# Kernel optimization log

Hardware: AMD Instinct MI355X
Metric: run time of the kernel (lower is better)

Reference implementation:

```python
import jax, jax.numpy as jnp
import numpy as np

L_MAX = 6
R = 1
IN_IRREPS  = [(256,0),(128,1),(128,2),(64,3),(64,4),(64,5),(64,6)]
HID_IRREPS = [(64,0),(64,1),(64,2),(32,3),(32,4),(32,5),(32,6)]
N_SCALARS = 64
N_GATES = sum(m for m, l in HID_IRREPS if l > 0)  # 256
PRE_IRREPS = [(N_SCALARS,0),(N_GATES,0)] + [(m,l) for m,l in HID_IRREPS if l > 0]
OUT_IRREPS = [(R,l) for l in range(L_MAX+1)]

def _dim(irr):
    return sum(m*(2*l+1) for m, l in irr)

def _wsize(in_irr, out_irr):
    mul_in = {l: m for m, l in in_irr}
    return sum(mul_in[l]*mo for mo, l in out_irr)

def e3linear(x, wflat, in_irr, out_irr):
    # block-diagonal per-irrep linear with e3nn 1/sqrt(fan_in) normalization
    B = x.shape[0]
    blocks = {}
    off = 0
    for mul, l in in_irr:
        d = mul*(2*l+1)
        blocks[l] = (x[:, off:off+d].reshape(B, mul, 2*l+1), mul)
        off += d
    outs = []
    woff = 0
    for mul_out, l in out_irr:
        xb, mul_in = blocks[l]
        w = wflat[woff:woff+mul_in*mul_out].reshape(mul_in, mul_out)
        woff += mul_in*mul_out
        y = jnp.einsum('bim,io->bom', xb, w) * (1.0/np.sqrt(mul_in))
        outs.append(y.reshape(B, mul_out*(2*l+1)))
    return jnp.concatenate(outs, axis=1)

def gate(z):
    # z = [scalars 64x0e | gates 256x0e | gated l>0 irreps]
    s = jax.nn.silu(z[:, :N_SCALARS])
    g = jax.nn.sigmoid(z[:, N_SCALARS:N_SCALARS+N_GATES])
    x = z[:, N_SCALARS+N_GATES:]
    outs = [s]
    goff = 0
    xoff = 0
    for mul, l in HID_IRREPS:
        if l == 0:
            continue
        m = 2*l+1
        xb = x[:, xoff:xoff+mul*m].reshape(-1, mul, m)
        outs.append((xb * g[:, goff:goff+mul, None]).reshape(-1, mul*m))
        goff += mul
        xoff += mul*m
    return jnp.concatenate(outs, axis=1)

def _forward(v_raw, w1, w2, w3, w4):
    x = gate(e3linear(v_raw, w1, IN_IRREPS, PRE_IRREPS))
    x = gate(e3linear(x, w2, HID_IRREPS, PRE_IRREPS))
    x = gate(e3linear(x, w3, HID_IRREPS, PRE_IRREPS))
    c = e3linear(x, w4, HID_IRREPS, OUT_IRREPS)  # [B, 49]
    B = c.shape[0]
    segs = []
    off = 0
    for l in range(L_MAX+1):
        m = 2*l+1
        seg = c[:, off:off+R*m].reshape(B, R, m).transpose(0, 2, 1)  # (B, m, R)
        segs.append(seg)
        off += R*m
    return jnp.concatenate(segs, axis=1)  # (B, 49, R)

def setup_inputs():
    key = jax.random.key(0)
    ks = jax.random.split(key, 5)
    B = 16384
    return {
        "v_raw": jax.random.normal(ks[0], (B, _dim(IN_IRREPS)), jnp.float32),
        "w1": jax.random.normal(ks[1], (_wsize(IN_IRREPS, PRE_IRREPS),), jnp.float32),
        "w2": jax.random.normal(ks[2], (_wsize(HID_IRREPS, PRE_IRREPS),), jnp.float32),
        "w3": jax.random.normal(ks[3], (_wsize(HID_IRREPS, PRE_IRREPS),), jnp.float32),
        "w4": jax.random.normal(ks[4], (_wsize(HID_IRREPS, OUT_IRREPS),), jnp.float32),
    }

def reference(v_raw, w1, w2, w3, w4):
    return _forward(v_raw, w1, w2, w3, w4)
```

## Files before the change

### kernel.cpp

```cpp
#include <hip/hip_runtime.h>
#include <cstddef>


typedef _Float16 half8 __attribute__((ext_vector_type(8)));
typedef _Float16 half4 __attribute__((ext_vector_type(4)));
typedef float    f32x4 __attribute__((ext_vector_type(4)));
typedef float    fvec4 __attribute__((ext_vector_type(4)));
typedef unsigned int u32x4 __attribute__((ext_vector_type(4)));

#define B_ROWS   16
#define IN_DIM   3840
#define OUT_COLS 49
#define GP  264
#define HSP 72

#define OFF_G1  0
#define OFF_G2  4224
#define OFF_G3  8448
#define OFF_HS1 12672
#define OFF_HS2 13824
#define SMEM_ELTS 14976

#define P2BASE 106496
#define P3BASE 139264

__global__ __launch_bounds__(256) void prep_weights(
    const float* __restrict__ w1, const float* __restrict__ w2,
    const float* __restrict__ w3, _Float16* __restrict__ packed)
{
  static const int K_[24]    = {256,256,128,128,64,64,64,64,  64,64,64,64,32,32,32,32,
                                64,64,64,64,32,32,32,32};
  static const int N_[24]    = {64,256,64,64,32,32,32,32,  64,256,64,64,32,32,32,32,
                                64,256,64,64,32,32,32,32};
  static const int woff_[24] = {0,16384,81920,90112,98304,100352,102400,104448,
                                0,4096,20480,24576,28672,29696,30720,31744,
                                0,4096,20480,24576,28672,29696,30720,31744};
  static const int poff_[24] = {0,16384,81920,90112,98304,100352,102400,104448,
                                106496,110592,126976,131072,135168,136192,137216,138240,
                                139264,143360,159744,163840,167936,168960,169984,171008};
  const int g = blockIdx.x * 256 + threadIdx.x;
  int bi = 0;
#pragma unroll
  for (int i = 1; i < 24; ++i) if (g * 8 >= poff_[i]) bi = i;
  const float* w = (bi < 8) ? w1 : ((bi < 16) ? w2 : w3);
  const int rel8 = g - poff_[bi] / 8;
  const int lane = rel8 & 63;
  const int fi   = rel8 >> 6;
  const int K = K_[bi], N = N_[bi];
  const int KF = K >> 5;
  const int kf = fi % KF;
  const int mt = fi / KF;
  const int k0 = kf * 32 + (lane >> 4) * 8;
  const int o  = mt * 16 + (lane & 15);
  const float scale = 1.0f / sqrtf((float)K);
  half8 vv;
#pragma unroll
  for (int j = 0; j < 8; ++j)
    vv[j] = (_Float16)(w[woff_[bi] + (size_t)(k0 + j) * N + o] * scale);
  *(half8*)(packed + (size_t)g * 8) = vv;
}

template<int L> struct CP {
  static constexpr int TWOL1 = 2 * L + 1;
  static constexpr int K1  = (L <= 2) ? 128 : 64;
  static constexpr int N1  = (L <= 2) ? 64  : 32;
  static constexpr int KF1 = K1 / 32;
  static constexpr int KF2 = N1 / 32;
  static constexpr int MT  = N1 / 16;
  static constexpr int INOFF = (L==1)?256:(L==2)?640:(L==3)?1280:(L==4)?1728:(L==5)?2304:3008;
  static constexpr int P1    = (L==1)?81920:(L==2)?90112:(L==3)?98304:(L==4)?100352:(L==5)?102400:104448;
  static constexpr int P2R   = (L==1)?20480:(L==2)?24576:(L==3)?28672:(L==4)?29696:(L==5)?30720:31744;
  static constexpr int GO    = (L==1)?0:(L==2)?64:(L==3)?128:(L==4)?160:(L==5)?192:224;
  static constexpr int W4O   = (L==1)?64:(L==2)?128:(L==3)?192:(L==4)?224:(L==5)?256:288;
  static constexpr float SCALE = (N1 == 64) ? 0.125f : 0.17677669529663687f;
};

__device__ __forceinline__ unsigned pack2(float x, float y)
{
  const unsigned short lo = __builtin_bit_cast(unsigned short, (_Float16)x);
  const unsigned short hi = __builtin_bit_cast(unsigned short, (_Float16)y);
  return ((unsigned)hi << 16) | (unsigned)lo;
}

template<int MT>
__device__ __forceinline__ void exchange(const unsigned (&p)[MT][2],
                                         half8 (&bv)[MT / 2])
{
  const int lane  = threadIdx.x & 63;
  const int addrA = (((lane & 15) + ((lane & 16) << 1)) << 2);
  const int addrB = addrA + 64;
  const bool useHi = (lane & 32) != 0;
#pragma unroll
  for (int h = 0; h < MT / 2; ++h) {
    const int a0 = __builtin_amdgcn_ds_bpermute(addrA, (int)p[2 * h][0]);
    const int a1 = __builtin_amdgcn_ds_bpermute(addrA, (int)p[2 * h][1]);
    const int a2 = __builtin_amdgcn_ds_bpermute(addrA, (int)p[2 * h + 1][0]);
    const int a3 = __builtin_amdgcn_ds_bpermute(addrA, (int)p[2 * h + 1][1]);
    const int b0 = __builtin_amdgcn_ds_bpermute(addrB, (int)p[2 * h][0]);
    const int b1 = __builtin_amdgcn_ds_bpermute(addrB, (int)p[2 * h][1]);
    const int b2 = __builtin_amdgcn_ds_bpermute(addrB, (int)p[2 * h + 1][0]);
    const int b3 = __builtin_amdgcn_ds_bpermute(addrB, (int)p[2 * h + 1][1]);
    u32x4 w;
    w[0] = (unsigned)(useHi ? a2 : a0);
    w[1] = (unsigned)(useHi ? a3 : a1);
    w[2] = (unsigned)(useHi ? b2 : b0);
    w[3] = (unsigned)(useHi ? b3 : b1);
    bv[h] = __builtin_bit_cast(half8, w);
  }
}

template<int L>
__device__ __forceinline__ void unit_load(const float* __restrict__ vraw,
                                          int b0, int ct, float (&rg)[CP<L>::KF1 * 8])
{
  using P = CP<L>;
  const int lane = threadIdx.x & 63;
  const int col  = lane & 15;
  const int quad = lane >> 4;
  const int c = ct * 16 + col;
  const int b = c / P::TWOL1;
  const int m = c - b * P::TWOL1;
  const float* base = vraw + (size_t)(b0 + b) * IN_DIM + P::INOFF + m
                    + (size_t)(quad * 8) * P::TWOL1;
#pragma unroll
  for (int kf = 0; kf < P::KF1; ++kf)
#pragma unroll
    for (int j = 0; j < 8; ++j)
      rg[kf * 8 + j] = base[(size_t)(kf * 32 + j) * P::TWOL1];
}

template<int L>
__device__ __forceinline__ void unit_compute(
    const float (&rg)[CP<L>::KF1 * 8], const _Float16* __restrict__ pk,
    const _Float16* G1, const _Float16* G2, const _Float16* G3,
    const float* __restrict__ w4, float* __restrict__ out, int b0, int ct)
{
  using P = CP<L>;
  const int lane = threadIdx.x & 63;
  const int col  = lane & 15;
  const int quad = lane >> 4;
  const int c = ct * 16 + col;
  const int b = c / P::TWOL1;
  const int m = c - b * P::TWOL1;
  half8 bf[P::KF1];
#pragma unroll
  for (int kf = 0; kf < P::KF1; ++kf)
#pragma unroll
    for (int j = 0; j < 8; ++j) bf[kf][j] = (_Float16)rg[kf * 8 + j];

  unsigned p1[P::MT][2];
#pragma unroll
  for (int mt = 0; mt < P::MT; ++mt) {
    f32x4 acc = {0.f, 0.f, 0.f, 0.f};
#pragma unroll
    for (int kf = 0; kf < P::KF1; ++kf) {
      const half8 av = *(const half8*)(pk + P::P1 + (size_t)((mt * P::KF1 + kf) * 64 + lane) * 8);
      acc = __builtin_amdgcn_mfma_f32_16x16x32_f16(av, bf[kf], acc, 0, 0, 0);
    }
    const int o0 = mt * 16 + quad * 4;
    const half4 g4 = *(const half4*)(G1 + b * GP + P::GO + o0);
    p1[mt][0] = pack2(acc[0] * (float)g4[0], acc[1] * (float)g4[1]);
    p1[mt][1] = pack2(acc[2] * (float)g4[2], acc[3] * (float)g4[3]);
  }
  half8 bv2[P::KF2];
  exchange<P::MT>(p1, bv2);

  unsigned p2[P::MT][2];
#pragma unroll
  for (int mt = 0; mt < P::MT; ++mt) {
    f32x4 acc = {0.f, 0.f, 0.f, 0.f};
#pragma unroll
    for (int kf = 0; kf < P::KF2; ++kf) {
      const half8 av = *(const half8*)(pk + P2BASE + P::P2R + (size_t)((mt * P::KF2 + kf) * 64 + lane) * 8);
      acc = __builtin_amdgcn_mfma_f32_16x16x32_f16(av, bv2[kf], acc, 0, 0, 0);
    }
    const int o0 = mt * 16 + quad * 4;
    const half4 g4 = *(const half4*)(G2 + b * GP + P::GO + o0);
    p2[mt][0] = pack2(acc[0] * (float)g4[0], acc[1] * (float)g4[1]);
    p2[mt][1] = pack2(acc[2] * (float)g4[2], acc[3] * (float)g4[3]);
  }
  half8 bv3[P::KF2];
  exchange<P::MT>(p2, bv3);

  float s = 0.f;
#pragma unroll
  for (int mt = 0; mt < P::MT; ++mt) {
    f32x4 acc = {0.f, 0.f, 0.f, 0.f};
#pragma unroll
    for (int kf = 0; kf < P::KF2; ++kf) {
      const half8 av = *(const half8*)(pk + P3BASE + P::P2R + (size_t)((mt * P::KF2 + kf) * 64 + lane) * 8);
      acc = __builtin_amdgcn_mfma_f32_16x16x32_f16(av, bv3[kf], acc, 0, 0, 0);
    }
    const int o0 = mt * 16 + quad * 4;
    const half4 g4 = *(const half4*)(G3 + b * GP + P::GO + o0);
#pragma unroll
    for (int r = 0; r < 4; ++r)
      s += acc[r] * (float)g4[r] * w4[P::W4O + o0 + r];
  }
  s += __shfl_xor(s, 16, 64);
  s += __shfl_xor(s, 32, 64);
  if (quad == 0)
    out[(size_t)(b0 + b) * OUT_COLS + L * L + m] = s * P::SCALE;
}

template<int L, int CT0, int NCT>
__device__ __forceinline__ void run_chain(
    const float* __restrict__ vraw, const _Float16* __restrict__ pk,
    const _Float16* G1, const _Float16* G2, const _Float16* G3,
    const float* __restrict__ w4, float* __restrict__ out, int b0)
{
  float rg[2][CP<L>::KF1 * 8];
  unit_load<L>(vraw, b0, CT0, rg[0]);
#pragma unroll
  for (int u = 0; u < NCT; ++u) {
    if (u + 1 < NCT) unit_load<L>(vraw, b0, CT0 + u + 1, rg[(u + 1) & 1]);
    unit_compute<L>(rg[u & 1], pk, G1, G2, G3, w4, out, b0, CT0 + u);
  }
}

template<int L, int CT0, int NCT>
__device__ __forceinline__ void run_chain_pre(
    const float* __restrict__ vraw, const _Float16* __restrict__ pk,
    const _Float16* G1, const _Float16* G2, const _Float16* G3,
    const float* __restrict__ w4, float* __restrict__ out, int b0,
    const float (&pre)[CP<L>::KF1 * 8])
{
  float rg[2][CP<L>::KF1 * 8];
#pragma unroll
  for (int i = 0; i < CP<L>::KF1 * 8; ++i) rg[0][i] = pre[i];
#pragma unroll
  for (int u = 0; u < NCT; ++u) {
    if (u + 1 < NCT) unit_load<L>(vraw, b0, CT0 + u + 1, rg[(u + 1) & 1]);
    unit_compute<L>(rg[u & 1], pk, G1, G2, G3, w4, out, b0, CT0 + u);
  }
}

__device__ __forceinline__ void load_scal_frags(const float* __restrict__ vraw,
                                                int b0, half8 (&sf)[8])
{
  const int lane = threadIdx.x & 63;
  const int col  = lane & 15;
  const int quad = lane >> 4;
  const float* base = vraw + (size_t)(b0 + col) * IN_DIM + quad * 8;
#pragma unroll
  for (int kf = 0; kf < 8; ++kf) {
    const fvec4 a = *(const fvec4*)(base + kf * 32);
    const fvec4 b2 = *(const fvec4*)(base + kf * 32 + 4);
#pragma unroll
    for (int j = 0; j < 4; ++j) { sf[kf][j] = (_Float16)a[j]; sf[kf][4 + j] = (_Float16)b2[j]; }
  }
}

__device__ __forceinline__ void scal_L1(const half8 (&sf)[8],
    const _Float16* __restrict__ pk, _Float16* Hs1, _Float16* G1v)
{
  const int lane = threadIdx.x & 63;
  const int wv   = threadIdx.x >> 6;
  const int col  = lane & 15;
  const int quad = lane >> 4;
  {
    f32x4 acc = {0.f, 0.f, 0.f, 0.f};
#pragma unroll
    for (int kf = 0; kf < 8; ++kf) {
      const half8 av = *(const half8*)(pk + (size_t)((wv * 8 + kf) * 64 + lane) * 8);
      acc = __builtin_amdgcn_mfma_f32_16x16x32_f16(av, sf[kf], acc, 0, 0, 0);
    }
    const int o0 = wv * 16 + quad * 4;
    half4 h;
#pragma unroll
    for (int r = 0; r < 4; ++r) { const float z = acc[r]; h[r] = (_Float16)(z / (1.f + __expf(-z))); }
    *(half4*)(Hs1 + col * HSP + o0) = h;
  }
#pragma unroll
  for (int t = 0; t < 4; ++t) {
    const int mt = wv * 4 + t;
    f32x4 acc = {0.f, 0.f, 0.f, 0.f};
#pragma unroll
    for (int kf = 0; kf < 8; ++kf) {
      const half8 av = *(const half8*)(pk + 16384 + (size_t)((mt * 8 + kf) * 64 + lane) * 8);
      acc = __builtin_amdgcn_mfma_f32_16x16x32_f16(av, sf[kf], acc, 0, 0, 0);
    }
    const int o0 = mt * 16 + quad * 4;
    half4 g;
#pragma unroll
    for (int r = 0; r < 4; ++r) g[r] = (_Float16)(1.f / (1.f + __expf(-acc[r])));
    *(half4*)(G1v + col * GP + o0) = g;
  }
}

__device__ __forceinline__ void scal_mid(const _Float16* HsIn,
    const _Float16* __restrict__ pkS, const _Float16* __restrict__ pkG,
    _Float16* HsOut, _Float16* Gv)
{
  const int lane = threadIdx.x & 63;
  const int wv   = threadIdx.x >> 6;
  const int col  = lane & 15;
  const int quad = lane >> 4;
  half8 bf[2];
#pragma unroll
  for (int kf = 0; kf < 2; ++kf)
    bf[kf] = *(const half8*)(HsIn + col * HSP + kf * 32 + quad * 8);
  {
    f32x4 acc = {0.f, 0.f, 0.f, 0.f};
#pragma unroll
    for (int kf = 0; kf < 2; ++kf) {
      const half8 av = *(const half8*)(pkS + (size_t)((wv * 2 + kf) * 64 + lane) * 8);
      acc = __builtin_amdgcn_mfma_f32_16x16x32_f16(av, bf[kf], acc, 0, 0, 0);
    }
    const int o0 = wv * 16 + quad * 4;
    half4 h;
#pragma unroll
    for (int r = 0; r < 4; ++r) { const float z = acc[r]; h[r] = (_Float16)(z / (1.f + __expf(-z))); }
    *(half4*)(HsOut + col * HSP + o0) = h;
  }
#pragma unroll
  for (int t = 0; t < 4; ++t) {
    const int mt = wv * 4 + t;
    f32x4 acc = {0.f, 0.f, 0.f, 0.f};
#pragma unroll
    for (int kf = 0; kf < 2; ++kf) {
      const half8 av = *(const half8*)(pkG + (size_t)((mt * 2 + kf) * 64 + lane) * 8);
      acc = __builtin_amdgcn_mfma_f32_16x16x32_f16(av, bf[kf], acc, 0, 0, 0);
    }
    const int o0 = mt * 16 + quad * 4;
    half4 g;
#pragma unroll
    for (int r = 0; r < 4; ++r) g[r] = (_Float16)(1.f / (1.f + __expf(-acc[r])));
    *(half4*)(Gv + col * GP + o0) = g;
  }
}

__device__ __forceinline__ void scal_last(const _Float16* Hs2,
    const _Float16* __restrict__ pkS, const _Float16* __restrict__ pkG,
    _Float16* G3v, const float* __restrict__ w4, float* __restrict__ out, int b0)
{
  const int lane = threadIdx.x & 63;
  const int wv   = threadIdx.x >> 6;
  const int col  = lane & 15;
  const int quad = lane >> 4;
  half8 bf[2];
#pragma unroll
  for (int kf = 0; kf < 2; ++kf)
    bf[kf] = *(const half8*)(Hs2 + col * HSP + kf * 32 + quad * 8);
  if (wv == 0) {
    float s = 0.f;
#pragma unroll
    for (int mt = 0; mt < 4; ++mt) {
      f32x4 acc = {0.f, 0.f, 0.f, 0.f};
#pragma unroll
      for (int kf = 0; kf < 2; ++kf) {
        const half8 av = *(const half8*)(pkS + (size_t)((mt * 2 + kf) * 64 + lane) * 8);
        acc = __builtin_amdgcn_mfma_f32_16x16x32_f16(av, bf[kf], acc, 0, 0, 0);
      }
      const int o0 = mt * 16 + quad * 4;
#pragma unroll
      for (int r = 0; r < 4; ++r) {
        const float z = acc[r];
        s += (z / (1.f + __expf(-z))) * w4[o0 + r];
      }
    }
    s += __shfl_xor(s, 16, 64);
    s += __shfl_xor(s, 32, 64);
    if (quad == 0) out[(size_t)(b0 + col) * OUT_COLS] = s * 0.125f;
  } else {
    const int t0 = (wv == 1) ? 0 : (wv == 2) ? 6 : 11;
    const int tn = (wv == 1) ? 6 : 5;
    for (int t = 0; t < tn; ++t) {
      const int mt = t0 + t;
      f32x4 acc = {0.f, 0.f, 0.f, 0.f};
#pragma unroll
      for (int kf = 0; kf < 2; ++kf) {
        const half8 av = *(const half8*)(pkG + (size_t)((mt * 2 + kf) * 64 + lane) * 8);
        acc = __builtin_amdgcn_mfma_f32_16x16x32_f16(av, bf[kf], acc, 0, 0, 0);
      }
      const int o0 = mt * 16 + quad * 4;
      half4 g;
#pragma unroll
      for (int r = 0; r < 4; ++r) g[r] = (_Float16)(1.f / (1.f + __expf(-acc[r])));
      *(half4*)(G3v + col * GP + o0) = g;
    }
  }
}

__global__ __launch_bounds__(256, 2) void fused_decoder(
    const float* __restrict__ vraw, const float* __restrict__ w4,
    const _Float16* __restrict__ pk, float* __restrict__ out)
{
  __shared__ __align__(16) _Float16 smem[SMEM_ELTS];
  _Float16* G1  = smem + OFF_G1;
  _Float16* G2  = smem + OFF_G2;
  _Float16* G3  = smem + OFF_G3;
  _Float16* Hs1 = smem + OFF_HS1;
  _Float16* Hs2 = smem + OFF_HS2;
  const int wv = threadIdx.x >> 6;
  const int b0 = blockIdx.x * B_ROWS;

  half8 sf[8];
  load_scal_frags(vraw, b0, sf);

  float pre[32];
  if (wv == 0)      unit_load<2>(vraw, b0, 0, reinterpret_cast<float(&)[32]>(pre));
  else if (wv == 1) unit_load<1>(vraw, b0, 0, reinterpret_cast<float(&)[32]>(pre));
  else if (wv == 2) unit_load<6>(vraw, b0, 0, reinterpret_cast<float(&)[16]>(pre));
  else              unit_load<5>(vraw, b0, 0, reinterpret_cast<float(&)[16]>(pre));

  scal_L1(sf, pk, Hs1, G1);
  __syncthreads();
  scal_mid(Hs1, pk + P2BASE, pk + P2BASE + 4096, Hs2, G2);
  __syncthreads();
  scal_last(Hs2, pk + P3BASE, pk + P3BASE + 4096, G3, w4, out, b0);
  __syncthreads();

  if (wv == 0) {
    run_chain_pre<2, 0, 5>(vraw, pk, G1, G2, G3, w4, out, b0,
                           reinterpret_cast<float(&)[32]>(pre));
    run_chain<3, 0, 4>(vraw, pk, G1, G2, G3, w4, out, b0);
  } else if (wv == 1) {
    run_chain_pre<1, 0, 3>(vraw, pk, G1, G2, G3, w4, out, b0,
                           reinterpret_cast<float(&)[32]>(pre));
    run_chain<3, 4, 3>(vraw, pk, G1, G2, G3, w4, out, b0);
    run_chain<4, 0, 5>(vraw, pk, G1, G2, G3, w4, out, b0);
  } else if (wv == 2) {
    run_chain_pre<6, 0, 13>(vraw, pk, G1, G2, G3, w4, out, b0,
                            reinterpret_cast<float(&)[16]>(pre));
    run_chain<4, 5, 1>(vraw, pk, G1, G2, G3, w4, out, b0);
  } else {
    run_chain_pre<5, 0, 11>(vraw, pk, G1, G2, G3, w4, out, b0,
                            reinterpret_cast<float(&)[16]>(pre));
    run_chain<4, 6, 3>(vraw, pk, G1, G2, G3, w4, out, b0);
  }
}

extern "C" void kernel_launch(void* const* d_in, const int* in_sizes, int n_in,
                              void* d_out, int out_size, void* d_ws, size_t ws_size,
                              hipStream_t stream)
{
  (void)in_sizes; (void)n_in; (void)out_size; (void)ws_size;
  const float* vraw = (const float*)d_in[0];
  const float* w1   = (const float*)d_in[1];
  const float* w2   = (const float*)d_in[2];
  const float* w3   = (const float*)d_in[3];
  const float* w4   = (const float*)d_in[4];
  float* out = (float*)d_out;
  _Float16* packed = (_Float16*)d_ws;

  prep_weights<<<84, 256, 0, stream>>>(w1, w2, w3, packed);
  fused_decoder<<<16384 / B_ROWS, 256, 0, stream>>>(vraw, w4, packed, out);
}
```

Measured before the change: 385.3 us.

## Use 16x16x16 MFMA for layers 2-3 to drop cross-lane bpermute exchange

Layers 2 and 3 (and the scalar paths) switch from the 16x16x32 f16 MFMA to the 16x16x16 variant, whose B-operand layout matches the C-output layout. The gated output of one layer can then feed the next MFMA directly, with no ds_bpermute shuffle between them. The weight prep kernel packs w2/w3 in the matching K=16 fragment layout. The cost is twice as many MFMA instructions for these layers, each with half the K depth.

```diff
diff --git a/kernel.cpp b/kernel.cpp
--- a/kernel.cpp
+++ b/kernel.cpp
@@ -6,7 +6,6 @@
 typedef _Float16 half4 __attribute__((ext_vector_type(4)));
 typedef float    f32x4 __attribute__((ext_vector_type(4)));
 typedef float    fvec4 __attribute__((ext_vector_type(4)));
-typedef unsigned int u32x4 __attribute__((ext_vector_type(4)));
 
 #define B_ROWS   16
 #define IN_DIM   3840
@@ -44,19 +43,36 @@
   for (int i = 1; i < 24; ++i) if (g * 8 >= poff_[i]) bi = i;
   const float* w = (bi < 8) ? w1 : ((bi < 16) ? w2 : w3);
   const int rel8 = g - poff_[bi] / 8;
-  const int lane = rel8 & 63;
-  const int fi   = rel8 >> 6;
   const int K = K_[bi], N = N_[bi];
-  const int KF = K >> 5;
-  const int kf = fi % KF;
-  const int mt = fi / KF;
-  const int k0 = kf * 32 + (lane >> 4) * 8;
-  const int o  = mt * 16 + (lane & 15);
   const float scale = 1.0f / sqrtf((float)K);
   half8 vv;
-#pragma unroll
-  for (int j = 0; j < 8; ++j)
-    vv[j] = (_Float16)(w[woff_[bi] + (size_t)(k0 + j) * N + o] * scale);
+  if (bi < 8) {
+    const int lane = rel8 & 63;
+    const int fi   = rel8 >> 6;
+    const int KF = K >> 5;
+    const int kf = fi % KF;
+    const int mt = fi / KF;
+    const int k0 = kf * 32 + (lane >> 4) * 8;
+    const int o  = mt * 16 + (lane & 15);
+#pragma unroll
+    for (int j = 0; j < 8; ++j)
+      vv[j] = (_Float16)(w[woff_[bi] + (size_t)(k0 + j) * N + o] * scale);
+  } else {
+    const int f  = rel8 >> 5;
+    const int lp = (rel8 & 31) << 1;
+    const int KF16 = K >> 4;
+    const int ks = f % KF16;
+    const int mt = f / KF16;
+#pragma unroll
+    for (int t = 0; t < 2; ++t) {
+      const int l  = lp + t;
+      const int i0 = ks * 16 + (l >> 4) * 4;
+      const int o  = mt * 16 + (l & 15);
+#pragma unroll
+      for (int j = 0; j < 4; ++j)
+        vv[t * 4 + j] = (_Float16)(w[woff_[bi] + (size_t)(i0 + j) * N + o] * scale);
+    }
+  }
   *(half8*)(packed + (size_t)g * 8) = vv;
 }
 
@@ -65,7 +81,6 @@
   static constexpr int K1  = (L <= 2) ? 128 : 64;
   static constexpr int N1  = (L <= 2) ? 64  : 32;
   static constexpr int KF1 = K1 / 32;
-  static constexpr int KF2 = N1 / 32;
   static constexpr int MT  = N1 / 16;
   static constexpr int INOFF = (L==1)?256:(L==2)?640:(L==3)?1280:(L==4)?1728:(L==5)?2304:3008;
   static constexpr int P1    = (L==1)?81920:(L==2)?90112:(L==3)?98304:(L==4)?100352:(L==5)?102400:104448;
@@ -75,40 +90,6 @@
   static constexpr float SCALE = (N1 == 64) ? 0.125f : 0.17677669529663687f;
 };
 
-__device__ __forceinline__ unsigned pack2(float x, float y)
-{
-  const unsigned short lo = __builtin_bit_cast(unsigned short, (_Float16)x);
-  const unsigned short hi = __builtin_bit_cast(unsigned short, (_Float16)y);
-  return ((unsigned)hi << 16) | (unsigned)lo;
-}
-
-template<int MT>
-__device__ __forceinline__ void exchange(const unsigned (&p)[MT][2],
-                                         half8 (&bv)[MT / 2])
-{
-  const int lane  = threadIdx.x & 63;
-  const int addrA = (((lane & 15) + ((lane & 16) << 1)) << 2);
-  const int addrB = addrA + 64;
-  const bool useHi = (lane & 32) != 0;
-#pragma unroll
-  for (int h = 0; h < MT / 2; ++h) {
-    const int a0 = __builtin_amdgcn_ds_bpermute(addrA, (int)p[2 * h][0]);
-    const int a1 = __builtin_amdgcn_ds_bpermute(addrA, (int)p[2 * h][1]);
-    const int a2 = __builtin_amdgcn_ds_bpermute(addrA, (int)p[2 * h + 1][0]);
-    const int a3 = __builtin_amdgcn_ds_bpermute(addrA, (int)p[2 * h + 1][1]);
-    const int b0 = __builtin_amdgcn_ds_bpermute(addrB, (int)p[2 * h][0]);
-    const int b1 = __builtin_amdgcn_ds_bpermute(addrB, (int)p[2 * h][1]);
-    const int b2 = __builtin_amdgcn_ds_bpermute(addrB, (int)p[2 * h + 1][0]);
-    const int b3 = __builtin_amdgcn_ds_bpermute(addrB, (int)p[2 * h + 1][1]);
-    u32x4 w;
-    w[0] = (unsigned)(useHi ? a2 : a0);
-    w[1] = (unsigned)(useHi ? a3 : a1);
-    w[2] = (unsigned)(useHi ? b2 : b0);
-    w[3] = (unsigned)(useHi ? b3 : b1);
-    bv[h] = __builtin_bit_cast(half8, w);
-  }
-}
-
 template<int L>
 __device__ __forceinline__ void unit_load(const float* __restrict__ vraw,
                                           int b0, int ct, float (&rg)[CP<L>::KF1 * 8])
@@ -148,7 +129,7 @@
 #pragma unroll
     for (int j = 0; j < 8; ++j) bf[kf][j] = (_Float16)rg[kf * 8 + j];
 
-  unsigned p1[P::MT][2];
+  half4 ph1[P::MT];
 #pragma unroll
   for (int mt = 0; mt < P::MT; ++mt) {
     f32x4 acc = {0.f, 0.f, 0.f, 0.f};
@@ -159,37 +140,37 @@
     }
     const int o0 = mt * 16 + quad * 4;
     const half4 g4 = *(const half4*)(G1 + b * GP + P::GO + o0);
-    p1[mt][0] = pack2(acc[0] * (float)g4[0], acc[1] * (float)g4[1]);
-    p1[mt][1] = pack2(acc[2] * (float)g4[2], acc[3] * (float)g4[3]);
-  }
-  half8 bv2[P::KF2];
-  exchange<P::MT>(p1, bv2);
-
-  unsigned p2[P::MT][2];
+    half4 h;
+#pragma unroll
+    for (int r = 0; r < 4; ++r) h[r] = (_Float16)(acc[r] * (float)g4[r]);
+    ph1[mt] = h;
+  }
+
+  half4 ph2[P::MT];
 #pragma unroll
   for (int mt = 0; mt < P::MT; ++mt) {
     f32x4 acc = {0.f, 0.f, 0.f, 0.f};
 #pragma unroll
-    for (int kf = 0; kf < P::KF2; ++kf) {
-      const half8 av = *(const half8*)(pk + P2BASE + P::P2R + (size_t)((mt * P::KF2 + kf) * 64 + lane) * 8);
-      acc = __builtin_amdgcn_mfma_f32_16x16x32_f16(av, bv2[kf], acc, 0, 0, 0);
+    for (int ks = 0; ks < P::MT; ++ks) {
+      const half4 av = *(const half4*)(pk + P2BASE + P::P2R + (size_t)((mt * P::MT + ks) * 64 + lane) * 4);
+      acc = __builtin_amdgcn_mfma_f32_16x16x16f16(av, ph1[ks], acc, 0, 0, 0);
     }
     const int o0 = mt * 16 + quad * 4;
     const half4 g4 = *(const half4*)(G2 + b * GP + P::GO + o0);
-    p2[mt][0] = pack2(acc[0] * (float)g4[0], acc[1] * (float)g4[1]);
-    p2[mt][1] = pack2(acc[2] * (float)g4[2], acc[3] * (float)g4[3]);
-  }
-  half8 bv3[P::KF2];
-  exchange<P::MT>(p2, bv3);
+    half4 h;
+#pragma unroll
+    for (int r = 0; r < 4; ++r) h[r] = (_Float16)(acc[r] * (float)g4[r]);
+    ph2[mt] = h;
+  }
 
   float s = 0.f;
 #pragma unroll
   for (int mt = 0; mt < P::MT; ++mt) {
     f32x4 acc = {0.f, 0.f, 0.f, 0.f};
 #pragma unroll
-    for (int kf = 0; kf < P::KF2; ++kf) {
-      const half8 av = *(const half8*)(pk + P3BASE + P::P2R + (size_t)((mt * P::KF2 + kf) * 64 + lane) * 8);
-      acc = __builtin_amdgcn_mfma_f32_16x16x32_f16(av, bv3[kf], acc, 0, 0, 0);
+    for (int ks = 0; ks < P::MT; ++ks) {
+      const half4 av = *(const half4*)(pk + P3BASE + P::P2R + (size_t)((mt * P::MT + ks) * 64 + lane) * 4);
+      acc = __builtin_amdgcn_mfma_f32_16x16x16f16(av, ph2[ks], acc, 0, 0, 0);
     }
     const int o0 = mt * 16 + quad * 4;
     const half4 g4 = *(const half4*)(G3 + b * GP + P::GO + o0);
@@ -296,16 +277,16 @@
   const int wv   = threadIdx.x >> 6;
   const int col  = lane & 15;
   const int quad = lane >> 4;
-  half8 bf[2];
-#pragma unroll
-  for (int kf = 0; kf < 2; ++kf)
-    bf[kf] = *(const half8*)(HsIn + col * HSP + kf * 32 + quad * 8);
+  half4 bf4[4];
+#pragma unroll
+  for (int ks = 0; ks < 4; ++ks)
+    bf4[ks] = *(const half4*)(HsIn + col * HSP + ks * 16 + quad * 4);
   {
     f32x4 acc = {0.f, 0.f, 0.f, 0.f};
 #pragma unroll
-    for (int kf = 0; kf < 2; ++kf) {
-      const half8 av = *(const half8*)(pkS + (size_t)((wv * 2 + kf) * 64 + lane) * 8);
-      acc = __builtin_amdgcn_mfma_f32_16x16x32_f16(av, bf[kf], acc, 0, 0, 0);
+    for (int ks = 0; ks < 4; ++ks) {
+      const half4 av = *(const half4*)(pkS + (size_t)((wv * 4 + ks) * 64 + lane) * 4);
+      acc = __builtin_amdgcn_mfma_f32_16x16x16f16(av, bf4[ks], acc, 0, 0, 0);
     }
     const int o0 = wv * 16 + quad * 4;
     half4 h;
@@ -318,9 +299,9 @@
     const int mt = wv * 4 + t;
     f32x4 acc = {0.f, 0.f, 0.f, 0.f};
 #pragma unroll
-    for (int kf = 0; kf < 2; ++kf) {
-      const half8 av = *(const half8*)(pkG + (size_t)((mt * 2 + kf) * 64 + lane) * 8);
-      acc = __builtin_amdgcn_mfma_f32_16x16x32_f16(av, bf[kf], acc, 0, 0, 0);
+    for (int ks = 0; ks < 4; ++ks) {
+      const half4 av = *(const half4*)(pkG + (size_t)((mt * 4 + ks) * 64 + lane) * 4);
+      acc = __builtin_amdgcn_mfma_f32_16x16x16f16(av, bf4[ks], acc, 0, 0, 0);
     }
     const int o0 = mt * 16 + quad * 4;
     half4 g;
@@ -338,19 +319,19 @@
   const int wv   = threadIdx.x >> 6;
   const int col  = lane & 15;
   const int quad = lane >> 4;
-  half8 bf[2];
-#pragma unroll
-  for (int kf = 0; kf < 2; ++kf)
-    bf[kf] = *(const half8*)(Hs2 + col * HSP + kf * 32 + quad * 8);
+  half4 bf4[4];
+#pragma unroll
+  for (int ks = 0; ks < 4; ++ks)
+    bf4[ks] = *(const half4*)(Hs2 + col * HSP + ks * 16 + quad * 4);
   if (wv == 0) {
     float s = 0.f;
 #pragma unroll
     for (int mt = 0; mt < 4; ++mt) {
       f32x4 acc = {0.f, 0.f, 0.f, 0.f};
 #pragma unroll
-      for (int kf = 0; kf < 2; ++kf) {
-        const half8 av = *(const half8*)(pkS + (size_t)((mt * 2 + kf) * 64 + lane) * 8);
-        acc = __builtin_amdgcn_mfma_f32_16x16x32_f16(av, bf[kf], acc, 0, 0, 0);
+      for (int ks = 0; ks < 4; ++ks) {
+        const half4 av = *(const half4*)(pkS + (size_t)((mt * 4 + ks) * 64 + lane) * 4);
+        acc = __builtin_amdgcn_mfma_f32_16x16x16f16(av, bf4[ks], acc, 0, 0, 0);
       }
       const int o0 = mt * 16 + quad * 4;
 #pragma unroll
@@ -369,9 +350,9 @@
       const int mt = t0 + t;
       f32x4 acc = {0.f, 0.f, 0.f, 0.f};
 #pragma unroll
-      for (int kf = 0; kf < 2; ++kf) {
-        const half8 av = *(const half8*)(pkG + (size_t)((mt * 2 + kf) * 64 + lane) * 8);
-        acc = __builtin_amdgcn_mfma_f32_16x16x32_f16(av, bf[kf], acc, 0, 0, 0);
+      for (int ks = 0; ks < 4; ++ks) {
+        const half4 av = *(const half4*)(pkG + (size_t)((mt * 4 + ks) * 64 + lane) * 4);
+        acc = __builtin_amdgcn_mfma_f32_16x16x16f16(av, bf4[ks], acc, 0, 0, 0);
       }
       const int o0 = mt * 16 + quad * 4;
       half4 g;
```

After: 388.2 us. About the same (+0.8%).
